# Performance work log

Measured on AMD Instinct MI355X. Metric: run time of the kernel, lower is better.

## Reference

```python
import jax, jax.numpy as jnp
import numpy as np

B, L, DM = 8, 1024, 1024
H, P, N, K = 32, 64, 128, 4   # nheads, headdim, d_state, d_conv
DI = H * P                    # d_inner = expand * d_model = 2048
DXBC = DI + 2 * N             # conv channels = 2304
DINP = 2 * DI + 2 * N + H     # in_proj width = 4404
ED = 2048                     # embed_dim

def setup_inputs():
    key = jax.random.key(0)
    ks = jax.random.split(key, 10)
    s = lambda i, shape, scale=0.02: jax.random.normal(ks[i], shape, jnp.float32) * scale
    return {
        "bert_out": jax.random.normal(ks[0], (B, L, 1024), jnp.float32),
        "w_pb": s(1, (1024, DM)), "b_pb": jnp.zeros((DM,), jnp.float32),
        "w_in": s(2, (DM, DINP)),
        "conv_w": s(3, (DXBC, K), 0.2), "conv_b": jnp.zeros((DXBC,), jnp.float32),
        "dt_bias": jax.random.uniform(ks[4], (H,), jnp.float32, -4.0, 0.0),
        "A_log": jnp.log(jnp.arange(1, H + 1, dtype=jnp.float32)),
        "D": jnp.ones((H,), jnp.float32),
        "norm_w": jnp.ones((DI,), jnp.float32),
        "w_outp": s(5, (DI, DM)),
        "w_attn": s(6, (DM, 1)), "b_attn": jnp.zeros((1,), jnp.float32),
        "w_emb": s(7, (DM, ED)), "b_emb": jnp.zeros((ED,), jnp.float32),
    }

def reference(bert_out, w_pb, b_pb, w_in, conv_w, conv_b, dt_bias, A_log, D,
              norm_w, w_outp, w_attn, b_attn, w_emb, b_emb):
    x = bert_out @ w_pb + b_pb                          # [B,L,DM] proj_bert
    # ---- Mamba2 ----
    zxbcdt = x @ w_in                                   # [B,L,DINP]
    z, xBC, dt = jnp.split(zxbcdt, [DI, DI + DXBC], axis=-1)
    # causal depthwise conv1d (kernel K) + SiLU
    xp = jnp.pad(xBC, ((0, 0), (K - 1, 0), (0, 0)))
    xBC = sum(xp[:, k:k + L, :] * conv_w[:, k] for k in range(K)) + conv_b
    xBC = jax.nn.silu(xBC)
    xs, Bm, Cm = jnp.split(xBC, [DI, DI + N], axis=-1)  # [B,L,DI],[B,L,N],[B,L,N]
    xs = xs.reshape(B, L, H, P)
    dt = jax.nn.softplus(dt + dt_bias)                  # [B,L,H]
    dA = jnp.exp(dt * (-jnp.exp(A_log)))                # [B,L,H]
    def step(h, inp):
        dA_t, dt_t, B_t, C_t, x_t = inp
        h = h * dA_t[:, :, None, None] + jnp.einsum('bh,bn,bhp->bhpn', dt_t, B_t, x_t)
        return h, jnp.einsum('bhpn,bn->bhp', h, C_t)
    h0 = jnp.zeros((B, H, P, N), x.dtype)
    _, ys = jax.lax.scan(step, h0, (dA.transpose(1, 0, 2), dt.transpose(1, 0, 2),
                                    Bm.transpose(1, 0, 2), Cm.transpose(1, 0, 2),
                                    xs.transpose(1, 0, 2, 3)))
    y = ys.transpose(1, 0, 2, 3) + D[None, None, :, None] * xs   # skip term
    y = y.reshape(B, L, DI) * jax.nn.silu(z)                     # gated
    y = y * jax.lax.rsqrt(jnp.mean(y * y, axis=-1, keepdims=True) + 1e-5) * norm_w
    emb = y @ w_outp                                             # [B,L,DM]
    # ---- attention pooling ----
    w = jax.nn.softmax(emb @ w_attn + b_attn, axis=1)            # [B,L,1]
    pooled = (emb * w).sum(axis=1)                               # [B,DM]
    # dropout is identity in eval mode
    return pooled @ w_emb + b_emb                                # [B,ED]
```

## Files before the change

kernel.cpp:

```cpp
#include <hip/hip_runtime.h>
#include <hip/hip_bf16.h>
#include <math.h>

#define B_    8
#define L_    1024
#define DM_   1024
#define H_    32
#define P_    64
#define NS_   128
#define DI_   2048
#define DXBC_ 2304
#define DINP_ 4384
#define ED_   2048

typedef __attribute__((ext_vector_type(8))) short bf8_t;
typedef __attribute__((ext_vector_type(8))) unsigned short u16x8;
typedef __attribute__((ext_vector_type(4))) float f4_t;

__device__ __forceinline__ float silu_f(float x) { return x / (1.f + __expf(-x)); }

__device__ __forceinline__ unsigned short f2bf(float x) {
    unsigned u = __float_as_uint(x);
    unsigned r = u + 0x7fffu + ((u >> 16) & 1u);
    return (unsigned short)(r >> 16);
}
__device__ __forceinline__ float bf2f(unsigned short h) {
    return __uint_as_float(((unsigned)h) << 16);
}

__global__ __launch_bounds__(256) void convw_k(
    const float* __restrict__ W, unsigned short* __restrict__ hi,
    unsigned short* __restrict__ lo, int K, int N, int Npad)
{
    size_t e = (size_t)blockIdx.x * 256 + threadIdx.x;
    if (e >= (size_t)K * Npad) return;
    int n = (int)(e % Npad), k = (int)(e / Npad);
    float v = (n < N) ? W[(size_t)k * N + n] : 0.f;
    unsigned short h = f2bf(v);
    unsigned short l = f2bf(v - bf2f(h));
    int nt = n >> 7, r = n & 127, kt = k >> 5, c = k & 31;
    size_t dst = ((size_t)(nt * (K >> 5) + kt) << 12) + (r << 5) + c;
    hi[dst] = h; lo[dst] = l;
}

template<bool CHECK_N>
__global__ __launch_bounds__(256, 2) void bgemm_k(
    const float* __restrict__ A, const unsigned short* __restrict__ Whi,
    const unsigned short* __restrict__ Wlo, float* __restrict__ C,
    const float* __restrict__ bias, int M, int N, int K, int ldc)
{
    __shared__ unsigned short Ah[128 * 40], Al[128 * 40];
    __shared__ unsigned short Bh[128 * 40], Bl[128 * 40];
    const int tid = threadIdx.x;
    const int m0 = blockIdx.y * 128, n0 = blockIdx.x * 128;
    const int lane = tid & 63;
    const int wv = tid >> 6;
    const int wr = wv >> 1, wc = wv & 1;
    const int l15 = lane & 15, l4 = lane >> 4;
    const int KT = K >> 5;

    f4_t acc[4][4];
#pragma unroll
    for (int i = 0; i < 4; i++)
#pragma unroll
        for (int j = 0; j < 4; j++) acc[i][j] = (f4_t){0.f, 0.f, 0.f, 0.f};

    const int ar = tid >> 2;
    const int ac = (tid & 3) * 8;
    const int wrow = tid >> 1;
    const int wcol = (tid & 1) * 16;

    for (int kt = 0; kt < KT; ++kt) {
        const int k0 = kt * 32;
        const float* Ap0 = A + (size_t)(m0 + ar) * K + k0 + ac;
        const float* Ap1 = Ap0 + (size_t)64 * K;
        float4 a00 = *(const float4*)Ap0, a01 = *(const float4*)(Ap0 + 4);
        float4 a10 = *(const float4*)Ap1, a11 = *(const float4*)(Ap1 + 4);
        const unsigned short* Whp = Whi + (((size_t)(blockIdx.x * KT + kt)) << 12);
        const unsigned short* Wlp = Wlo + (((size_t)(blockIdx.x * KT + kt)) << 12);
        u16x8 whv0 = *(const u16x8*)(Whp + (wrow << 5) + wcol);
        u16x8 whv1 = *(const u16x8*)(Whp + (wrow << 5) + wcol + 8);
        u16x8 wlv0 = *(const u16x8*)(Wlp + (wrow << 5) + wcol);
        u16x8 wlv1 = *(const u16x8*)(Wlp + (wrow << 5) + wcol + 8);

        __syncthreads();
        {
            float av0[8] = {a00.x, a00.y, a00.z, a00.w, a01.x, a01.y, a01.z, a01.w};
            float av1[8] = {a10.x, a10.y, a10.z, a10.w, a11.x, a11.y, a11.z, a11.w};
            u16x8 vh0, vl0, vh1, vl1;
#pragma unroll
            for (int j = 0; j < 8; j++) {
                unsigned short h0 = f2bf(av0[j]);
                vh0[j] = h0; vl0[j] = f2bf(av0[j] - bf2f(h0));
                unsigned short h1 = f2bf(av1[j]);
                vh1[j] = h1; vl1[j] = f2bf(av1[j] - bf2f(h1));
            }
            *(u16x8*)&Ah[ar * 40 + ac] = vh0;
            *(u16x8*)&Al[ar * 40 + ac] = vl0;
            *(u16x8*)&Ah[(ar + 64) * 40 + ac] = vh1;
            *(u16x8*)&Al[(ar + 64) * 40 + ac] = vl1;
            *(u16x8*)&Bh[wrow * 40 + wcol]     = whv0;
            *(u16x8*)&Bh[wrow * 40 + wcol + 8] = whv1;
            *(u16x8*)&Bl[wrow * 40 + wcol]     = wlv0;
            *(u16x8*)&Bl[wrow * 40 + wcol + 8] = wlv1;
        }
        __syncthreads();

        bf8_t afh[4], afl[4], bfh[4], bfl[4];
#pragma unroll
        for (int i = 0; i < 4; i++) {
            int off = (wr * 64 + i * 16 + l15) * 40 + l4 * 8;
            afh[i] = *(const bf8_t*)&Ah[off];
            afl[i] = *(const bf8_t*)&Al[off];
        }
#pragma unroll
        for (int j = 0; j < 4; j++) {
            int off = (wc * 64 + j * 16 + l15) * 40 + l4 * 8;
            bfh[j] = *(const bf8_t*)&Bh[off];
            bfl[j] = *(const bf8_t*)&Bl[off];
        }
#pragma unroll
        for (int i = 0; i < 4; i++)
#pragma unroll
            for (int j = 0; j < 4; j++) {
                acc[i][j] = __builtin_amdgcn_mfma_f32_16x16x32_bf16(afh[i], bfh[j], acc[i][j], 0, 0, 0);
                acc[i][j] = __builtin_amdgcn_mfma_f32_16x16x32_bf16(afl[i], bfh[j], acc[i][j], 0, 0, 0);
                acc[i][j] = __builtin_amdgcn_mfma_f32_16x16x32_bf16(afh[i], bfl[j], acc[i][j], 0, 0, 0);
            }
    }

#pragma unroll
    for (int j = 0; j < 4; j++) {
        int col = n0 + wc * 64 + j * 16 + l15;
        bool ok = !CHECK_N || (col < N);
        float bv = 0.f;
        if (bias && ok) bv = bias[col];
        if (ok) {
#pragma unroll
            for (int i = 0; i < 4; i++) {
                int rbase = m0 + wr * 64 + i * 16 + l4 * 4;
#pragma unroll
                for (int r = 0; r < 4; r++)
                    C[(size_t)(rbase + r) * ldc + col] = acc[i][j][r] + bv;
            }
        }
    }
}

template<bool CHECK_N>
__global__ __launch_bounds__(256, 2) void sgemm_k(
    const float* __restrict__ A, const float* __restrict__ Bw,
    float* __restrict__ C, const float* __restrict__ bias,
    int M, int N, int K, int ldb, int ldc)
{
    __shared__ float As[16][128];
    __shared__ float Bs[16][128];
    const int tid = threadIdx.x;
    const int m0 = blockIdx.y * 128;
    const int n0 = blockIdx.x * 128;
    const int tx = tid & 15;
    const int ty = tid >> 4;
    const int arr = tid >> 1;
    const int acc_ = (tid & 1) * 8;
    const int bk = tid >> 5;
    const int bn = (tid & 31) * 4;

    float acc[8][8];
#pragma unroll
    for (int i = 0; i < 8; i++)
#pragma unroll
        for (int j = 0; j < 8; j++) acc[i][j] = 0.f;

    for (int k0 = 0; k0 < K; k0 += 16) {
        float4 a0 = *(const float4*)(A + (size_t)(m0 + arr) * K + k0 + acc_);
        float4 a1 = *(const float4*)(A + (size_t)(m0 + arr) * K + k0 + acc_ + 4);
        float4 b0, b1;
        if (!CHECK_N || (n0 + bn) < N) {
            b0 = *(const float4*)(Bw + (size_t)(k0 + bk) * ldb + n0 + bn);
            b1 = *(const float4*)(Bw + (size_t)(k0 + bk + 8) * ldb + n0 + bn);
        } else {
            b0 = make_float4(0.f, 0.f, 0.f, 0.f);
            b1 = make_float4(0.f, 0.f, 0.f, 0.f);
        }
        __syncthreads();
        As[acc_ + 0][arr] = a0.x; As[acc_ + 1][arr] = a0.y;
        As[acc_ + 2][arr] = a0.z; As[acc_ + 3][arr] = a0.w;
        As[acc_ + 4][arr] = a1.x; As[acc_ + 5][arr] = a1.y;
        As[acc_ + 6][arr] = a1.z; As[acc_ + 7][arr] = a1.w;
        *(float4*)&Bs[bk][bn]     = b0;
        *(float4*)&Bs[bk + 8][bn] = b1;
        __syncthreads();
#pragma unroll
        for (int kk = 0; kk < 16; kk++) {
            float4 av0 = *(const float4*)&As[kk][ty * 8];
            float4 av1 = *(const float4*)&As[kk][ty * 8 + 4];
            float4 bv0 = *(const float4*)&Bs[kk][tx * 4];
            float4 bv1 = *(const float4*)&Bs[kk][64 + tx * 4];
            float a_[8] = {av0.x, av0.y, av0.z, av0.w, av1.x, av1.y, av1.z, av1.w};
            float b_[8] = {bv0.x, bv0.y, bv0.z, bv0.w, bv1.x, bv1.y, bv1.z, bv1.w};
#pragma unroll
            for (int i = 0; i < 8; i++)
#pragma unroll
                for (int j = 0; j < 8; j++) acc[i][j] += a_[i] * b_[j];
        }
    }
    float4 bb0 = make_float4(0.f, 0.f, 0.f, 0.f), bb1 = bb0;
    if (bias) {
        if (!CHECK_N || (n0 + tx * 4) < N)      bb0 = *(const float4*)(bias + n0 + tx * 4);
        if (!CHECK_N || (n0 + 64 + tx * 4) < N) bb1 = *(const float4*)(bias + n0 + 64 + tx * 4);
    }
#pragma unroll
    for (int i = 0; i < 8; i++) {
        size_t row = (size_t)(m0 + ty * 8 + i) * ldc + n0;
        if (!CHECK_N || (n0 + tx * 4) < N) {
            float4 v = make_float4(acc[i][0] + bb0.x, acc[i][1] + bb0.y,
                                   acc[i][2] + bb0.z, acc[i][3] + bb0.w);
            *(float4*)(C + row + tx * 4) = v;
        }
        if (!CHECK_N || (n0 + 64 + tx * 4) < N) {
            float4 v = make_float4(acc[i][4] + bb1.x, acc[i][5] + bb1.y,
                                   acc[i][6] + bb1.z, acc[i][7] + bb1.w);
            *(float4*)(C + row + 64 + tx * 4) = v;
        }
    }
}

__global__ __launch_bounds__(256) void dt_k(
    const float* __restrict__ zx, const float* __restrict__ dt_bias,
    const float* __restrict__ A_log, float* __restrict__ dtp, float* __restrict__ dAb)
{
    int e = blockIdx.x * 256 + threadIdx.x;
    int l = e & 1023;
    int h = (e >> 10) & 31;
    int b = e >> 15;
    float dtr = zx[((size_t)b * L_ + l) * DINP_ + (DI_ + DXBC_) + h];
    float u = dtr + dt_bias[h];
    float sp = (u > 20.f) ? u : log1pf(__expf(u));
    float da = __expf(-__expf(A_log[h]) * sp);
    size_t o = ((size_t)b * H_ + h) * L_ + l;
    dtp[o] = sp;
    dAb[o] = da;
}

__global__ __launch_bounds__(256) void stash_k(const float* __restrict__ zx, float* __restrict__ stash)
{
    int e = blockIdx.x * 256 + threadIdx.x;
    int c = e % DXBC_;
    int r = e / DXBC_;
    int k = r % 3;
    int bc = r / 3;
    int chunk = bc & 7;
    int b = bc >> 3;
    int t = chunk * 128 - 3 + k;
    float v = 0.f;
    if (t >= 0) v = zx[((size_t)b * L_ + t) * DINP_ + DI_ + c];
    stash[e] = v;
}

__global__ __launch_bounds__(256) void conv_k(
    float* __restrict__ zx, const float* __restrict__ cw,
    const float* __restrict__ cb, const float* __restrict__ stash)
{
    int tid = threadIdx.x;
    int cblk = blockIdx.x;
    int chunk = blockIdx.y;
    int b = blockIdx.z;
    int c = cblk * 256 + tid;
    float4 w = *(const float4*)(cw + (size_t)c * 4);
    float bias = cb[c];
    const float* st = stash + ((size_t)(b * 8 + chunk) * 3) * DXBC_ + c;
    float x0 = st[0], x1 = st[DXBC_], x2 = st[2 * DXBC_];
    int t0 = chunk * 128;
    size_t base = ((size_t)b * L_ + t0) * DINP_ + DI_ + c;
#pragma unroll 4
    for (int t = 0; t < 128; t++) {
        float xt = zx[base + (size_t)t * DINP_];
        float a = w.x * x0 + w.y * x1 + w.z * x2 + w.w * xt + bias;
        a = a / (1.f + __expf(-a));
        zx[base + (size_t)t * DINP_] = a;
        x0 = x1; x1 = x2; x2 = xt;
    }
}

__global__ __launch_bounds__(1024, 1) void scan_k(
    const float* __restrict__ zx, const float* __restrict__ dtp,
    const float* __restrict__ dAb, const float* __restrict__ Dp,
    float* __restrict__ ys)
{
    int bh = blockIdx.x;
    int b = bh >> 5, h = bh & 31;
    int tid = threadIdx.x;
    int lane = tid & 63;
    int gu = __builtin_amdgcn_readfirstlane(tid >> 6);
    int nbase = gu * 8;
    __shared__ float ypart[16][16][64];
    float hreg[8];
#pragma unroll
    for (int j = 0; j < 8; j++) hreg[j] = 0.f;
    float Dh = Dp[h];
    const float* dtrow = dtp + ((size_t)b * H_ + h) * L_;
    const float* darow = dAb + ((size_t)b * H_ + h) * L_;

    float4 pb0, pb1, pc0, pc1;
    float px, pdt, pda;
    {
        size_t row = (size_t)(b * L_) * DINP_;
        const float* Bp = zx + row + 2 * DI_ + nbase;
        pb0 = *(const float4*)Bp;
        pb1 = *(const float4*)(Bp + 4);
        pc0 = *(const float4*)(Bp + NS_);
        pc1 = *(const float4*)(Bp + NS_ + 4);
        px  = zx[row + DI_ + h * 64 + lane];
        pdt = dtrow[0];
        pda = darow[0];
    }

    for (int c0 = 0; c0 < L_; c0 += 16) {
#pragma unroll
        for (int tt = 0; tt < 16; ++tt) {
            int t = c0 + tt;
            float4 b0 = pb0, b1 = pb1, cv0 = pc0, cv1 = pc1;
            float xv = px, dtv = pdt, dav = pda;
            if (t + 1 < L_) {
                size_t row2 = (size_t)(b * L_ + t + 1) * DINP_;
                const float* Bp = zx + row2 + 2 * DI_ + nbase;
                pb0 = *(const float4*)Bp;
                pb1 = *(const float4*)(Bp + 4);
                pc0 = *(const float4*)(Bp + NS_);
                pc1 = *(const float4*)(Bp + NS_ + 4);
                px  = zx[row2 + DI_ + h * 64 + lane];
                pdt = dtrow[t + 1];
                pda = darow[t + 1];
            }
            float u = dtv * xv;
            float yacc = 0.f;
            hreg[0] = hreg[0] * dav + u * b0.x; yacc += hreg[0] * cv0.x;
            hreg[1] = hreg[1] * dav + u * b0.y; yacc += hreg[1] * cv0.y;
            hreg[2] = hreg[2] * dav + u * b0.z; yacc += hreg[2] * cv0.z;
            hreg[3] = hreg[3] * dav + u * b0.w; yacc += hreg[3] * cv0.w;
            hreg[4] = hreg[4] * dav + u * b1.x; yacc += hreg[4] * cv1.x;
            hreg[5] = hreg[5] * dav + u * b1.y; yacc += hreg[5] * cv1.y;
            hreg[6] = hreg[6] * dav + u * b1.z; yacc += hreg[6] * cv1.z;
            hreg[7] = hreg[7] * dav + u * b1.w; yacc += hreg[7] * cv1.w;
            ypart[tt][gu][lane] = yacc;
        }
        __syncthreads();
        {
            int tsub = tid >> 6;
            int t = c0 + tsub;
            float v = 0.f;
#pragma unroll
            for (int w = 0; w < 16; w++) v += ypart[tsub][w][lane];
            size_t row = (size_t)(b * L_ + t) * DINP_;
            float xv = zx[row + DI_ + h * 64 + lane];
            ys[((size_t)b * L_ + t) * DI_ + h * 64 + lane] = v + Dh * xv;
        }
        __syncthreads();
    }
}

__global__ __launch_bounds__(256) void gate_norm_k(
    float* __restrict__ ys, const float* __restrict__ zx, const float* __restrict__ nw)
{
    int row = blockIdx.x;
    int tid = threadIdx.x;
    float* yr = ys + (size_t)row * DI_;
    const float* zr = zx + (size_t)row * DINP_;
    float4 v[2];
    float ss = 0.f;
#pragma unroll
    for (int i = 0; i < 2; i++) {
        int d = tid * 4 + i * 1024;
        float4 yv = *(const float4*)(yr + d);
        float4 zv = *(const float4*)(zr + d);
        v[i].x = yv.x * silu_f(zv.x);
        v[i].y = yv.y * silu_f(zv.y);
        v[i].z = yv.z * silu_f(zv.z);
        v[i].w = yv.w * silu_f(zv.w);
        ss += v[i].x * v[i].x + v[i].y * v[i].y + v[i].z * v[i].z + v[i].w * v[i].w;
    }
    __shared__ float red[256];
    red[tid] = ss;
    __syncthreads();
    for (int s = 128; s > 0; s >>= 1) {
        if (tid < s) red[tid] += red[tid + s];
        __syncthreads();
    }
    float scale = rsqrtf(red[0] / (float)DI_ + 1e-5f);
#pragma unroll
    for (int i = 0; i < 2; i++) {
        int d = tid * 4 + i * 1024;
        float4 nwv = *(const float4*)(nw + d);
        float4 o = make_float4(v[i].x * scale * nwv.x, v[i].y * scale * nwv.y,
                               v[i].z * scale * nwv.z, v[i].w * scale * nwv.w);
        *(float4*)(yr + d) = o;
    }
}

__global__ __launch_bounds__(256) void attnw_k(
    const float* __restrict__ emb, const float* __restrict__ wat,
    const float* __restrict__ batn, float* __restrict__ logits)
{
    int row = blockIdx.x * 4 + (threadIdx.x >> 6);
    int lane = threadIdx.x & 63;
    const float* er = emb + (size_t)row * DM_;
    float s = 0.f;
#pragma unroll
    for (int k = 0; k < 16; k++) s += er[lane + k * 64] * wat[lane + k * 64];
#pragma unroll
    for (int off = 32; off; off >>= 1) s += __shfl_down(s, off);
    if (lane == 0) logits[row] = s + batn[0];
}

__global__ __launch_bounds__(256) void softmax_k(
    const float* __restrict__ logits, float* __restrict__ wght, float* __restrict__ pooled)
{
    int b = blockIdx.x;
    int tid = threadIdx.x;
    __shared__ float red[256];
    float4 lv = *(const float4*)(logits + (size_t)b * L_ + tid * 4);
    float m = fmaxf(fmaxf(lv.x, lv.y), fmaxf(lv.z, lv.w));
    red[tid] = m;
    __syncthreads();
    for (int s = 128; s > 0; s >>= 1) {
        if (tid < s) red[tid] = fmaxf(red[tid], red[tid + s]);
        __syncthreads();
    }
    float bm = red[0];
    __syncthreads();
    float e0 = __expf(lv.x - bm), e1 = __expf(lv.y - bm);
    float e2 = __expf(lv.z - bm), e3 = __expf(lv.w - bm);
    red[tid] = e0 + e1 + e2 + e3;
    __syncthreads();
    for (int s = 128; s > 0; s >>= 1) {
        if (tid < s) red[tid] += red[tid + s];
        __syncthreads();
    }
    float inv = 1.f / red[0];
    *(float4*)(wght + (size_t)b * L_ + tid * 4) = make_float4(e0 * inv, e1 * inv, e2 * inv, e3 * inv);
    *(float4*)(pooled + (size_t)b * DM_ + tid * 4) = make_float4(0.f, 0.f, 0.f, 0.f);
}

__global__ __launch_bounds__(256) void pool_k(
    const float* __restrict__ emb, const float* __restrict__ wght, float* __restrict__ pooled)
{
    int b = blockIdx.x, dc = blockIdx.y, lc = blockIdx.z;
    int d = dc * 256 + threadIdx.x;
    const float* wr = wght + (size_t)b * L_ + lc * 64;
    float acc = 0.f;
#pragma unroll 4
    for (int lt = 0; lt < 64; lt++)
        acc += emb[((size_t)(b * L_ + lc * 64 + lt)) * DM_ + d] * wr[lt];
    atomicAdd(pooled + (size_t)b * DM_ + d, acc);
}

__global__ __launch_bounds__(256) void outp_k(
    const float* __restrict__ pooled, const float* __restrict__ wemb,
    const float* __restrict__ bemb, float* __restrict__ out)
{
    int ec = blockIdx.x, b = blockIdx.y;
    int tid = threadIdx.x;
    __shared__ float pl[DM_];
#pragma unroll
    for (int i = 0; i < 4; i++) pl[tid + i * 256] = pooled[(size_t)b * DM_ + tid + i * 256];
    __syncthreads();
    int e = ec * 256 + tid;
    float acc = bemb[e];
#pragma unroll 4
    for (int d = 0; d < DM_; d++) acc += pl[d] * wemb[(size_t)d * ED_ + e];
    out[(size_t)b * ED_ + e] = acc;
}

extern "C" void kernel_launch(void* const* d_in, const int* in_sizes, int n_in,
                              void* d_out, int out_size, void* d_ws, size_t ws_size,
                              hipStream_t stream)
{
    (void)in_sizes; (void)n_in; (void)out_size;
    const float* bert    = (const float*)d_in[0];
    const float* w_pb    = (const float*)d_in[1];
    const float* b_pb    = (const float*)d_in[2];
    const float* w_in    = (const float*)d_in[3];
    const float* conv_w  = (const float*)d_in[4];
    const float* conv_b  = (const float*)d_in[5];
    const float* dt_bias = (const float*)d_in[6];
    const float* A_log   = (const float*)d_in[7];
    const float* Dp      = (const float*)d_in[8];
    const float* norm_w  = (const float*)d_in[9];
    const float* w_outp  = (const float*)d_in[10];
    const float* w_attn  = (const float*)d_in[11];
    const float* b_attn  = (const float*)d_in[12];
    const float* w_emb   = (const float*)d_in[13];
    const float* b_emb   = (const float*)d_in[14];
    float* out = (float*)d_out;

    float* ws     = (float*)d_ws;
    float* zx     = ws;
    float* ys     = zx  + (size_t)8192 * 4384;
    float* xe     = ys  + (size_t)8192 * 2048;
    float* dtp    = xe  + (size_t)8192 * 1024;
    float* dAb    = dtp + 262144;
    float* stash  = dAb + 262144;
    float* logits = stash + 442368;
    float* wght   = logits + 8192;
    float* pooled = wght + 8192;
    float* fend   = pooled + 8192;

    size_t wpb_n = (size_t)8  * 32 * 4096;
    size_t win_n = (size_t)35 * 32 * 4096;
    size_t wop_n = (size_t)8  * 64 * 4096;
    unsigned short* wpb_h = (unsigned short*)ys;
    unsigned short* wpb_l = wpb_h + wpb_n;
    unsigned short* win_h = wpb_l + wpb_n;
    unsigned short* win_l = win_h + win_n;
    unsigned short* wop_h = (unsigned short*)zx;
    unsigned short* wop_l = wop_h + wop_n;

    size_t need_bytes = (size_t)((char*)fend - (char*)d_ws);
    bool use_mfma = ws_size >= need_bytes;

    if (use_mfma) {
        convw_k<<<(unsigned)(((size_t)1024 * 1024 + 255) / 256), 256, 0, stream>>>(
            w_pb, wpb_h, wpb_l, 1024, 1024, 1024);
        convw_k<<<(unsigned)(((size_t)1024 * 4480 + 255) / 256), 256, 0, stream>>>(
            w_in, win_h, win_l, 1024, 4384, 4480);
        bgemm_k<false><<<dim3(8, 64), 256, 0, stream>>>(bert, wpb_h, wpb_l, xe, b_pb,
                                                        8192, 1024, 1024, 1024);
        bgemm_k<true><<<dim3(35, 64), 256, 0, stream>>>(xe, win_h, win_l, zx, nullptr,
                                                        8192, 4384, 1024, 4384);
    } else {
        sgemm_k<false><<<dim3(8, 64), 256, 0, stream>>>(bert, w_pb, xe, b_pb,
                                                        8192, 1024, 1024, 1024, 1024);
        sgemm_k<true><<<dim3(35, 64), 256, 0, stream>>>(xe, w_in, zx, nullptr,
                                                        8192, 4384, 1024, 4384, 4384);
    }
    dt_k<<<1024, 256, 0, stream>>>(zx, dt_bias, A_log, dtp, dAb);
    stash_k<<<1728, 256, 0, stream>>>(zx, stash);
    conv_k<<<dim3(9, 8, 8), 256, 0, stream>>>(zx, conv_w, conv_b, stash);
    scan_k<<<256, 1024, 0, stream>>>(zx, dtp, dAb, Dp, ys);
    gate_norm_k<<<8192, 256, 0, stream>>>(ys, zx, norm_w);
    if (use_mfma) {
        convw_k<<<(unsigned)(((size_t)2048 * 1024 + 255) / 256), 256, 0, stream>>>(
            w_outp, wop_h, wop_l, 2048, 1024, 1024);
        bgemm_k<false><<<dim3(8, 64), 256, 0, stream>>>(ys, wop_h, wop_l, xe, nullptr,
                                                        8192, 1024, 2048, 1024);
    } else {
        sgemm_k<false><<<dim3(8, 64), 256, 0, stream>>>(ys, w_outp, xe, nullptr,
                                                        8192, 1024, 2048, 1024, 1024);
    }
    attnw_k<<<2048, 256, 0, stream>>>(xe, w_attn, b_attn, logits);
    softmax_k<<<8, 256, 0, stream>>>(logits, wght, pooled);
    pool_k<<<dim3(8, 4, 16), 256, 0, stream>>>(xe, wght, pooled);
    outp_k<<<dim3(8, 8), 256, 0, stream>>>(pooled, w_emb, b_emb, out);
}
```

Baseline: 1.063 ms.

## Stage scan inputs cooperatively in LDS with chunked prefetch

The selective-scan kernel no longer has every wave redundantly load B, C, x, dt and dA from global memory at each timestep. The block now loads 8 timesteps of these inputs into shared memory in one cooperative step, prefetching the next chunk into registers while it computes the current one. This reduces redundant global traffic and load latency on the serial recurrence. The cost is smaller chunks (8 instead of 16), so there are twice as many block-wide barriers, plus LDS reads on every step. The output accumulation is also split into two partial sums to shorten the dependency chain.

Measured after the change: 975.1 us. -8.2%, faster.

```diff
diff --git a/kernel.cpp b/kernel.cpp
--- a/kernel.cpp
+++ b/kernel.cpp
@@ -293,7 +293,10 @@
     int lane = tid & 63;
     int gu = __builtin_amdgcn_readfirstlane(tid >> 6);
     int nbase = gu * 8;
-    __shared__ float ypart[16][16][64];
+    __shared__ float ypart[8][16][64];
+    __shared__ float bcs[8][256];
+    __shared__ float xss[8][64];
+    __shared__ float dtda[2][8];
     float hreg[8];
 #pragma unroll
     for (int j = 0; j < 8; j++) hreg[j] = 0.f;
@@ -301,59 +304,73 @@
     const float* dtrow = dtp + ((size_t)b * H_ + h) * L_;
     const float* darow = dAb + ((size_t)b * H_ + h) * L_;
 
-    float4 pb0, pb1, pc0, pc1;
-    float px, pdt, pda;
+    const int st_t = tid >> 7;
+    const int st_j = (tid & 127) * 2;
+    const int sx_t = tid >> 6;
+    const int sx_ok = (sx_t < 8);
+
     {
-        size_t row = (size_t)(b * L_) * DINP_;
-        const float* Bp = zx + row + 2 * DI_ + nbase;
-        pb0 = *(const float4*)Bp;
-        pb1 = *(const float4*)(Bp + 4);
-        pc0 = *(const float4*)(Bp + NS_);
-        pc1 = *(const float4*)(Bp + NS_ + 4);
-        px  = zx[row + DI_ + h * 64 + lane];
-        pdt = dtrow[0];
-        pda = darow[0];
-    }
-
-    for (int c0 = 0; c0 < L_; c0 += 16) {
-#pragma unroll
-        for (int tt = 0; tt < 16; ++tt) {
-            int t = c0 + tt;
-            float4 b0 = pb0, b1 = pb1, cv0 = pc0, cv1 = pc1;
-            float xv = px, dtv = pdt, dav = pda;
-            if (t + 1 < L_) {
-                size_t row2 = (size_t)(b * L_ + t + 1) * DINP_;
-                const float* Bp = zx + row2 + 2 * DI_ + nbase;
-                pb0 = *(const float4*)Bp;
-                pb1 = *(const float4*)(Bp + 4);
-                pc0 = *(const float4*)(Bp + NS_);
-                pc1 = *(const float4*)(Bp + NS_ + 4);
-                px  = zx[row2 + DI_ + h * 64 + lane];
-                pdt = dtrow[t + 1];
-                pda = darow[t + 1];
+        size_t row = ((size_t)b * L_ + st_t) * DINP_;
+        float2 bc2 = *(const float2*)(zx + row + 2 * DI_ + st_j);
+        *(float2*)&bcs[st_t][st_j] = bc2;
+        if (sx_ok) {
+            size_t rowx = ((size_t)b * L_ + sx_t) * DINP_;
+            xss[sx_t][lane] = zx[rowx + DI_ + h * 64 + lane];
+        }
+        if (tid < 8)               dtda[0][tid] = dtrow[tid];
+        else if (tid < 16)         dtda[1][tid - 8] = darow[tid - 8];
+    }
+    __syncthreads();
+
+    float xout = 0.f;
+    for (int c0 = 0; c0 < L_; c0 += 8) {
+        float2 nbc; float nx = 0.f, nd = 0.f;
+        const bool pf = (c0 + 8) < L_;
+        if (pf) {
+            size_t row = ((size_t)b * L_ + c0 + 8 + st_t) * DINP_;
+            nbc = *(const float2*)(zx + row + 2 * DI_ + st_j);
+            if (sx_ok) {
+                size_t rowx = ((size_t)b * L_ + c0 + 8 + sx_t) * DINP_;
+                nx = zx[rowx + DI_ + h * 64 + lane];
             }
+            if (tid < 8)       nd = dtrow[c0 + 8 + tid];
+            else if (tid < 16) nd = darow[c0 + 8 + tid - 8];
+        }
+#pragma unroll
+        for (int tt = 0; tt < 8; ++tt) {
+            float dtv = dtda[0][tt];
+            float dav = dtda[1][tt];
+            float xv  = xss[tt][lane];
+            if (tt == gu) xout = xv;
+            float4 b0  = *(const float4*)&bcs[tt][nbase];
+            float4 b1  = *(const float4*)&bcs[tt][nbase + 4];
+            float4 cv0 = *(const float4*)&bcs[tt][128 + nbase];
+            float4 cv1 = *(const float4*)&bcs[tt][128 + nbase + 4];
             float u = dtv * xv;
-            float yacc = 0.f;
-            hreg[0] = hreg[0] * dav + u * b0.x; yacc += hreg[0] * cv0.x;
-            hreg[1] = hreg[1] * dav + u * b0.y; yacc += hreg[1] * cv0.y;
-            hreg[2] = hreg[2] * dav + u * b0.z; yacc += hreg[2] * cv0.z;
-            hreg[3] = hreg[3] * dav + u * b0.w; yacc += hreg[3] * cv0.w;
-            hreg[4] = hreg[4] * dav + u * b1.x; yacc += hreg[4] * cv1.x;
-            hreg[5] = hreg[5] * dav + u * b1.y; yacc += hreg[5] * cv1.y;
-            hreg[6] = hreg[6] * dav + u * b1.z; yacc += hreg[6] * cv1.z;
-            hreg[7] = hreg[7] * dav + u * b1.w; yacc += hreg[7] * cv1.w;
-            ypart[tt][gu][lane] = yacc;
-        }
-        __syncthreads();
-        {
-            int tsub = tid >> 6;
-            int t = c0 + tsub;
+            float ya = 0.f, yb = 0.f;
+            hreg[0] = hreg[0] * dav + u * b0.x; ya += hreg[0] * cv0.x;
+            hreg[1] = hreg[1] * dav + u * b0.y; yb += hreg[1] * cv0.y;
+            hreg[2] = hreg[2] * dav + u * b0.z; ya += hreg[2] * cv0.z;
+            hreg[3] = hreg[3] * dav + u * b0.w; yb += hreg[3] * cv0.w;
+            hreg[4] = hreg[4] * dav + u * b1.x; ya += hreg[4] * cv1.x;
+            hreg[5] = hreg[5] * dav + u * b1.y; yb += hreg[5] * cv1.y;
+            hreg[6] = hreg[6] * dav + u * b1.z; ya += hreg[6] * cv1.z;
+            hreg[7] = hreg[7] * dav + u * b1.w; yb += hreg[7] * cv1.w;
+            ypart[tt][gu][lane] = ya + yb;
+        }
+        __syncthreads();
+        if (gu < 8) {
+            int t = c0 + gu;
             float v = 0.f;
 #pragma unroll
-            for (int w = 0; w < 16; w++) v += ypart[tsub][w][lane];
-            size_t row = (size_t)(b * L_ + t) * DINP_;
-            float xv = zx[row + DI_ + h * 64 + lane];
-            ys[((size_t)b * L_ + t) * DI_ + h * 64 + lane] = v + Dh * xv;
+            for (int w = 0; w < 16; w++) v += ypart[gu][w][lane];
+            ys[((size_t)b * L_ + t) * DI_ + h * 64 + lane] = v + Dh * xout;
+        }
+        if (pf) {
+            *(float2*)&bcs[st_t][st_j] = nbc;
+            if (sx_ok) xss[sx_t][lane] = nx;
+            if (tid < 8)       dtda[0][tid] = nd;
+            else if (tid < 16) dtda[1][tid - 8] = nd;
         }
         __syncthreads();
     }
```
